# Kernel tuning notes

Hardware: AMD Instinct MI355X
Metric: run time of the kernel (lower is better)

The kernel has to match this reference:

```python
import jax, jax.numpy as jnp
import numpy as np
from jax import lax

N_NODES = 64; N_GROUPS = 16; GROUP_SIZE = 4
B = 256; L = 64; CNN_C = 32; GH = 128; DH = 128; OUT = 64
E1 = 262144; E2 = 32768
GROUP_NODES = jnp.arange(N_NODES).reshape(N_GROUPS, GROUP_SIZE)

PARAM_SHAPES = [
    ('conv_w3', (N_NODES, CNN_C, 3)), ('conv_b3', (N_NODES, CNN_C)),
    ('conv_w5', (N_NODES, CNN_C, 5)), ('conv_b5', (N_NODES, CNN_C)),
    ('conv_w7', (N_NODES, CNN_C, 7)), ('conv_b7', (N_NODES, CNN_C)),
    ('tconv_w3', (N_NODES, CNN_C, 3)), ('tconv_b3', (N_NODES, CNN_C)),
    ('tconv_w5', (N_NODES, CNN_C, 5)), ('tconv_b5', (N_NODES, CNN_C)),
    ('tconv_w7', (N_NODES, CNN_C, 7)), ('tconv_b7', (N_NODES, CNN_C)),
    ('ff_w', (N_NODES, 6 * CNN_C, GH)), ('ff_b', (N_NODES, GH)),
    ('lower_w', (GH, GH)), ('lower_b', (GH,)),
    ('upper_w', (GH, GH)), ('upper_b', (GH,)),
    ('agg_w', (N_GROUPS, GROUP_SIZE * GH, GH)), ('agg_b', (N_GROUPS, GH)),
    ('disc_w', (N_GROUPS, 2 * GH, DH)), ('disc_b', (N_GROUPS, DH)),
    ('fc_w', (N_GROUPS * DH, OUT)), ('fc_b', (OUT,)),
]


def setup_inputs() -> dict:
    key = jax.random.key(0)
    ks = jax.random.split(key, 6 + len(PARAM_SHAPES))
    d = {
        'x1': jax.random.normal(ks[0], (B * N_NODES, 4, L), jnp.float32),
        'x2': jax.random.normal(ks[1], (B * N_NODES, 4, L), jnp.float32),
        'edge_index1': jax.random.randint(ks[2], (2, E1), 0, B * N_NODES),
        'edge_index2': jax.random.randint(ks[3], (2, E1), 0, B * N_NODES),
        'group_edge_index1': jax.random.randint(ks[4], (2, E2), 0, B * N_GROUPS),
        'group_edge_index2': jax.random.randint(ks[5], (2, E2), 0, B * N_GROUPS),
    }
    for i, (name, shape) in enumerate(PARAM_SHAPES):
        d[name] = jax.random.normal(ks[6 + i], shape, jnp.float32) * 0.05
    return d


def _grouped_conv_max(x, w, b, pad):
    # x: [B, N, Lx] (one input channel per node), w: [N, C, k], b: [N, C]
    N, C, k = w.shape
    y = lax.conv_general_dilated(x, w.reshape(N * C, 1, k), (1,), [(pad, pad)],
                                 feature_group_count=N,
                                 dimension_numbers=('NCH', 'OIH', 'NCH'))
    y = y + b.reshape(1, N * C, 1)
    return y.max(axis=2).reshape(x.shape[0], N, C)  # max over time per channel


def _gcn(x, edge_index, W, bias):
    # PyG GCNConv: add self loops, symmetric D^-1/2 (A+I) D^-1/2 normalization
    n = x.shape[0]
    loops = jnp.arange(n)
    src = jnp.concatenate([edge_index[0], loops])
    dst = jnp.concatenate([edge_index[1], loops])
    deg = jax.ops.segment_sum(jnp.ones(src.shape[0], x.dtype), dst, n)
    dinv = jnp.where(deg > 0, lax.rsqrt(deg), 0.0)
    h = x @ W
    msg = h[src] * (dinv[src] * dinv[dst])[:, None]
    return jax.ops.segment_sum(msg, dst, n) + bias


def reference(x1, x2, edge_index1, edge_index2, group_edge_index1, group_edge_index2,
              conv_w3, conv_b3, conv_w5, conv_b5, conv_w7, conv_b7,
              tconv_w3, tconv_b3, tconv_w5, tconv_b5, tconv_w7, tconv_b7,
              ff_w, ff_b, lower_w, lower_b, upper_w, upper_b,
              agg_w, agg_b, disc_w, disc_b, fc_w, fc_b):
    def encode(x, ei, gei):
        xr = x.reshape(B, N_NODES, 4, L)  # row = b*N_NODES + n -> x[n::N] == xr[:, n]
        feats = jnp.concatenate([
            _grouped_conv_max(xr[:, :, 0, :], conv_w3, conv_b3, 1),
            _grouped_conv_max(xr[:, :, 0, :], conv_w5, conv_b5, 2),
            _grouped_conv_max(xr[:, :, 0, :], conv_w7, conv_b7, 3),
            _grouped_conv_max(xr[:, :, 1, :-2], tconv_w3, tconv_b3, 1),
            _grouped_conv_max(xr[:, :, 2, :-4], tconv_w5, tconv_b5, 2),
            _grouped_conv_max(xr[:, :, 3, :-6], tconv_w7, tconv_b7, 3),
        ], axis=2)  # [B, N, 6C]
        feats = jax.nn.relu(feats)
        h = jax.nn.relu(jnp.einsum('bnf,nfh->bnh', feats, ff_w) + ff_b)  # per-node Linear
        h = _gcn(h.reshape(B * N_NODES, GH), ei, lower_w, lower_b)
        hg = h.reshape(B, N_NODES, GH)[:, GROUP_NODES]  # [B, G, S, GH]
        hg = hg.reshape(B, N_GROUPS, GROUP_SIZE * GH)
        hg = jnp.einsum('bgf,gfh->bgh', hg, agg_w) + agg_b  # per-group aggregate Linear
        hg = _gcn(hg.reshape(B * N_GROUPS, GH), gei, upper_w, upper_b)
        return jax.nn.relu(hg).reshape(B, N_GROUPS, GH)

    h1 = encode(x1, edge_index1, group_edge_index1)
    h2 = encode(x2, edge_index2, group_edge_index2)
    d = jnp.concatenate([h1, h2], axis=2)  # [B, G, 2*GH]
    d = jax.nn.relu(jnp.einsum('bgf,gfd->bgd', d, disc_w) + disc_b)  # per-group disc fc
    return d.reshape(B, N_GROUPS * DH) @ fc_w + fc_b  # [B, OUT]
```

## Files before the change

kernel.cpp:

```cpp
#include <hip/hip_runtime.h>
#include <hip/hip_bf16.h>

namespace {

constexpr int Bn      = 256;
constexpr int NNODES  = 64;
constexpr int NGROUPS = 16;
constexpr int L       = 64;
constexpr int C       = 32;
constexpr int GH      = 128;
constexpr int E1      = 262144;
constexpr int E2      = 32768;
constexpr int NROWS   = Bn * NNODES;
constexpr int GROWS   = Bn * NGROUPS;
constexpr int XROW    = 296;

template<int K, int LX>
__device__ __forceinline__ void convmax2(const float* __restrict__ xin_al,
                                         const float* __restrict__ wpa,
                                         const float* __restrict__ wpb,
                                         float& ma, float& mb)
{
    constexpr int PAD = (K - 1) / 2;
    constexpr int OFF = 3 - PAD;
    float wa[K], wb[K];
    #pragma unroll
    for (int i = 0; i < K; ++i) { wa[i] = wpa[i]; wb[i] = wpb[i]; }
    ma = -3.0e38f; mb = -3.0e38f;
    #pragma unroll
    for (int p0 = 0; p0 < LX; p0 += 16) {
        float xw[24];
        #pragma unroll
        for (int q = 0; q < 6; ++q) {
            const float4 v = *(const float4*)(xin_al + p0 + q * 4);
            xw[q * 4 + 0] = v.x; xw[q * 4 + 1] = v.y;
            xw[q * 4 + 2] = v.z; xw[q * 4 + 3] = v.w;
        }
        #pragma unroll
        for (int p = 0; p < 16; p += 2) {
            if (p0 + p + 1 < LX) {
                float sa0 = 0.f, sb0 = 0.f, sa1 = 0.f, sb1 = 0.f;
                #pragma unroll
                for (int i = 0; i < K; ++i) {
                    const float xv0 = xw[p + OFF + i];
                    const float xv1 = xw[p + 1 + OFF + i];
                    sa0 = fmaf(wa[i], xv0, sa0);
                    sb0 = fmaf(wb[i], xv0, sb0);
                    sa1 = fmaf(wa[i], xv1, sa1);
                    sb1 = fmaf(wb[i], xv1, sb1);
                }
                ma = fmaxf(fmaxf(sa0, sa1), ma);
                mb = fmaxf(fmaxf(sb0, sb1), mb);
            }
        }
    }
}

__device__ __forceinline__ void conv6_ch0(
    const float* __restrict__ xin_al,
    const float* __restrict__ w3a, const float* __restrict__ w3b,
    const float* __restrict__ w5a, const float* __restrict__ w5b,
    const float* __restrict__ w7a, const float* __restrict__ w7b,
    float& m3a, float& m3b, float& m5a, float& m5b, float& m7a, float& m7b)
{
    float a3[3], b3[3], a5[5], b5[5], a7[7], b7[7];
    #pragma unroll
    for (int i = 0; i < 3; ++i) { a3[i] = w3a[i]; b3[i] = w3b[i]; }
    #pragma unroll
    for (int i = 0; i < 5; ++i) { a5[i] = w5a[i]; b5[i] = w5b[i]; }
    #pragma unroll
    for (int i = 0; i < 7; ++i) { a7[i] = w7a[i]; b7[i] = w7b[i]; }
    m3a = m3b = m5a = m5b = m7a = m7b = -3.0e38f;
    #pragma unroll
    for (int p0 = 0; p0 < 64; p0 += 16) {
        float xw[24];
        #pragma unroll
        for (int q = 0; q < 6; ++q) {
            const float4 v = *(const float4*)(xin_al + p0 + q * 4);
            xw[q * 4 + 0] = v.x; xw[q * 4 + 1] = v.y;
            xw[q * 4 + 2] = v.z; xw[q * 4 + 3] = v.w;
        }
        #pragma unroll
        for (int p = 0; p < 16; p += 2) {
            float s3a0 = 0.f, s3b0 = 0.f, s3a1 = 0.f, s3b1 = 0.f;
            #pragma unroll
            for (int i = 0; i < 3; ++i) {
                const float xv0 = xw[p + 2 + i], xv1 = xw[p + 3 + i];
                s3a0 = fmaf(a3[i], xv0, s3a0); s3b0 = fmaf(b3[i], xv0, s3b0);
                s3a1 = fmaf(a3[i], xv1, s3a1); s3b1 = fmaf(b3[i], xv1, s3b1);
            }
            m3a = fmaxf(fmaxf(s3a0, s3a1), m3a);
            m3b = fmaxf(fmaxf(s3b0, s3b1), m3b);
            float s5a0 = 0.f, s5b0 = 0.f, s5a1 = 0.f, s5b1 = 0.f;
            #pragma unroll
            for (int i = 0; i < 5; ++i) {
                const float xv0 = xw[p + 1 + i], xv1 = xw[p + 2 + i];
                s5a0 = fmaf(a5[i], xv0, s5a0); s5b0 = fmaf(b5[i], xv0, s5b0);
                s5a1 = fmaf(a5[i], xv1, s5a1); s5b1 = fmaf(b5[i], xv1, s5b1);
            }
            m5a = fmaxf(fmaxf(s5a0, s5a1), m5a);
            m5b = fmaxf(fmaxf(s5b0, s5b1), m5b);
            float s7a0 = 0.f, s7b0 = 0.f, s7a1 = 0.f, s7b1 = 0.f;
            #pragma unroll
            for (int i = 0; i < 7; ++i) {
                const float xv0 = xw[p + 0 + i], xv1 = xw[p + 1 + i];
                s7a0 = fmaf(a7[i], xv0, s7a0); s7b0 = fmaf(b7[i], xv0, s7b0);
                s7a1 = fmaf(a7[i], xv1, s7a1); s7b1 = fmaf(b7[i], xv1, s7b1);
            }
            m7a = fmaxf(fmaxf(s7a0, s7a1), m7a);
            m7b = fmaxf(fmaxf(s7b0, s7b1), m7b);
        }
    }
}

__global__ __launch_bounds__(256) void k_conv_feats(
    const float* __restrict__ x1, const float* __restrict__ x2,
    const float* __restrict__ w3,  const float* __restrict__ b3,
    const float* __restrict__ w5,  const float* __restrict__ b5,
    const float* __restrict__ w7,  const float* __restrict__ b7,
    const float* __restrict__ tw3, const float* __restrict__ tb3,
    const float* __restrict__ tw5, const float* __restrict__ tb5,
    const float* __restrict__ tw7, const float* __restrict__ tb7,
    float* __restrict__ feats)
{
    __shared__ float xs[16 * XROW];
    const int t = threadIdx.x;
    const int eb = blockIdx.x >> 10;
    const float* __restrict__ x = eb ? x2 : x1;
    const int row0 = (blockIdx.x & 1023) * 16;
    for (int idx = t; idx < 16 * 4 * 72; idx += 256) {
        const int r   = idx / 288;
        const int rem = idx - r * 288;
        const int c   = rem / 72;
        const int j   = rem - c * 72;
        const int l   = j - 3;
        float v = 0.f;
        if (l >= 0 && l < 64 - 2 * c)
            v = x[(size_t)(row0 + r) * 256 + c * 64 + l];
        xs[r * XROW + c * 72 + j] = v;
    }
    __syncthreads();

    const int rr  = t >> 4;
    const int cp  = t & 15;
    const int ch0 = cp * 2;
    const int row = row0 + rr;
    const int n   = row & (NNODES - 1);
    const int wc0 = n * C + ch0;
    const int wc1 = wc0 + 1;
    const float* xb0 = &xs[rr * XROW + 0 * 72];
    const float* xb1 = &xs[rr * XROW + 1 * 72];
    const float* xb2 = &xs[rr * XROW + 2 * 72];
    const float* xb3 = &xs[rr * XROW + 3 * 72];

    float* o = feats + (size_t)(eb * NROWS + row) * 192 + ch0;

    float m3a, m3b, m5a, m5b, m7a, m7b;
    conv6_ch0(xb0, w3 + wc0 * 3, w3 + wc1 * 3, w5 + wc0 * 5, w5 + wc1 * 5,
              w7 + wc0 * 7, w7 + wc1 * 7, m3a, m3b, m5a, m5b, m7a, m7b);
    *(float2*)(o + 0 * 32) = make_float2(fmaxf(m3a + b3[wc0], 0.f), fmaxf(m3b + b3[wc1], 0.f));
    *(float2*)(o + 1 * 32) = make_float2(fmaxf(m5a + b5[wc0], 0.f), fmaxf(m5b + b5[wc1], 0.f));
    *(float2*)(o + 2 * 32) = make_float2(fmaxf(m7a + b7[wc0], 0.f), fmaxf(m7b + b7[wc1], 0.f));

    float ma, mb;
    convmax2<3, 62>(xb1, tw3 + wc0 * 3, tw3 + wc1 * 3, ma, mb);
    *(float2*)(o + 3 * 32) = make_float2(fmaxf(ma + tb3[wc0], 0.f), fmaxf(mb + tb3[wc1], 0.f));
    convmax2<5, 60>(xb2, tw5 + wc0 * 5, tw5 + wc1 * 5, ma, mb);
    *(float2*)(o + 4 * 32) = make_float2(fmaxf(ma + tb5[wc0], 0.f), fmaxf(mb + tb5[wc1], 0.f));
    convmax2<7, 58>(xb3, tw7 + wc0 * 7, tw7 + wc1 * 7, ma, mb);
    *(float2*)(o + 5 * 32) = make_float2(fmaxf(ma + tb7[wc0], 0.f), fmaxf(mb + tb7[wc1], 0.f));
}

__global__ __launch_bounds__(256) void k_ff_lower(
    const float* __restrict__ feats, const float* __restrict__ ffw,
    const float* __restrict__ ffb, const float* __restrict__ lw,
    float* __restrict__ hw)
{
    const int nb = blockIdx.x >> 6;
    const int n  = blockIdx.x & 63;
    const int t  = threadIdx.x;
    const int o  = t & 127;
    const int rh = t >> 7;
    __shared__ float fs[16 * 192];
    __shared__ float h0s[16 * 128];
    {
        float4* d4 = (float4*)fs;
        for (int i = t; i < 16 * 48; i += 256) {
            const int r = i / 48, c4 = i - r * 48;
            d4[i] = *(const float4*)(feats + ((size_t)(nb * 16 + r) * 64 + n) * 192 + c4 * 4);
        }
    }
    __syncthreads();
    {
        const float* w = ffw + (size_t)n * 192 * 128 + o;
        float acc[8];
        #pragma unroll
        for (int r = 0; r < 8; ++r) acc[r] = 0.f;
        #pragma unroll 2
        for (int f = 0; f < 192; f += 4) {
            const float w0 = w[(f + 0) * 128];
            const float w1 = w[(f + 1) * 128];
            const float w2 = w[(f + 2) * 128];
            const float w3_ = w[(f + 3) * 128];
            #pragma unroll
            for (int r = 0; r < 8; ++r) {
                const float4 xv = *(const float4*)(fs + (rh * 8 + r) * 192 + f);
                acc[r] = fmaf(xv.x, w0, acc[r]);
                acc[r] = fmaf(xv.y, w1, acc[r]);
                acc[r] = fmaf(xv.z, w2, acc[r]);
                acc[r] = fmaf(xv.w, w3_, acc[r]);
            }
        }
        const float bias = ffb[n * 128 + o];
        #pragma unroll
        for (int r = 0; r < 8; ++r)
            h0s[(rh * 8 + r) * 128 + o] = fmaxf(acc[r] + bias, 0.f);
    }
    __syncthreads();
    {
        const float* w = lw + o;
        float acc[8];
        #pragma unroll
        for (int r = 0; r < 8; ++r) acc[r] = 0.f;
        #pragma unroll 2
        for (int f = 0; f < 128; f += 4) {
            const float w0 = w[(f + 0) * 128];
            const float w1 = w[(f + 1) * 128];
            const float w2 = w[(f + 2) * 128];
            const float w3_ = w[(f + 3) * 128];
            #pragma unroll
            for (int r = 0; r < 8; ++r) {
                const float4 xv = *(const float4*)(h0s + (rh * 8 + r) * 128 + f);
                acc[r] = fmaf(xv.x, w0, acc[r]);
                acc[r] = fmaf(xv.y, w1, acc[r]);
                acc[r] = fmaf(xv.z, w2, acc[r]);
                acc[r] = fmaf(xv.w, w3_, acc[r]);
            }
        }
        #pragma unroll
        for (int r = 0; r < 8; ++r) {
            const int row = nb * 16 + rh * 8 + r;
            hw[((size_t)row * 64 + n) * 128 + o] = acc[r];
        }
    }
}

__global__ __launch_bounds__(256) void k_gemm128(
    const float* __restrict__ X, const float* __restrict__ W,
    float* __restrict__ Y)
{
    const int r0 = blockIdx.x * 16;
    const int t  = threadIdx.x;
    const int o  = t & 127;
    const int rh = t >> 7;
    __shared__ float xs[16 * 128];
    {
        float4* d4 = (float4*)xs;
        const float4* s4 = (const float4*)(X + (size_t)r0 * 128);
        for (int i = t; i < 512; i += 256) d4[i] = s4[i];
    }
    __syncthreads();
    const float* w = W + o;
    float acc[8];
    #pragma unroll
    for (int r = 0; r < 8; ++r) acc[r] = 0.f;
    #pragma unroll 2
    for (int f = 0; f < 128; f += 4) {
        const float w0 = w[(f + 0) * 128];
        const float w1 = w[(f + 1) * 128];
        const float w2 = w[(f + 2) * 128];
        const float w3_ = w[(f + 3) * 128];
        #pragma unroll
        for (int r = 0; r < 8; ++r) {
            const float4 xv = *(const float4*)(xs + (rh * 8 + r) * 128 + f);
            acc[r] = fmaf(xv.x, w0, acc[r]);
            acc[r] = fmaf(xv.y, w1, acc[r]);
            acc[r] = fmaf(xv.z, w2, acc[r]);
            acc[r] = fmaf(xv.w, w3_, acc[r]);
        }
    }
    #pragma unroll
    for (int r = 0; r < 8; ++r)
        Y[(size_t)(r0 + rh * 8 + r) * 128 + o] = acc[r];
}

__global__ void k_zero_i(int* __restrict__ p, int n) {
    const int i = blockIdx.x * blockDim.x + threadIdx.x;
    if (i < n) p[i] = 0;
}
__global__ void k_hist_all(const int* __restrict__ ei0, const int* __restrict__ ei1,
                           const int* __restrict__ gei0, const int* __restrict__ gei1,
                           int* __restrict__ cnt1, int* __restrict__ cnt2)
{
    const int gid = blockIdx.x * blockDim.x + threadIdx.x;
    if (gid < 2 * E1) {
        const int eb = gid >= E1;
        const int le = gid - (eb ? E1 : 0);
        const int* ei = eb ? ei1 : ei0;
        atomicAdd(&cnt1[(eb ? NROWS : 0) + ei[E1 + le]], 1);
    } else {
        const int g2 = gid - 2 * E1;
        const int eb = g2 >= E2;
        const int le = g2 - (eb ? E2 : 0);
        const int* ei = eb ? gei1 : gei0;
        atomicAdd(&cnt2[(eb ? GROWS : 0) + ei[E2 + le]], 1);
    }
}
__global__ __launch_bounds__(256) void k_scan_bsum_all(
    const int* __restrict__ cnt1, const int* __restrict__ cnt2,
    int* __restrict__ bsum1, int* __restrict__ bsum2)
{
    const int blk = blockIdx.x, t = threadIdx.x;
    const int* cnt; int* bsum; int lblk;
    if (blk < 32) { cnt = cnt1; bsum = bsum1; lblk = blk; }
    else          { cnt = cnt2; bsum = bsum2; lblk = blk - 32; }
    const int4 v = ((const int4*)cnt)[lblk * 256 + t];
    int s = v.x + v.y + v.z + v.w;
    #pragma unroll
    for (int off = 32; off > 0; off >>= 1) s += __shfl_down(s, off);
    __shared__ int wsum[4];
    if ((t & 63) == 0) wsum[t >> 6] = s;
    __syncthreads();
    if (t == 0) bsum[lblk] = wsum[0] + wsum[1] + wsum[2] + wsum[3];
}
__global__ __launch_bounds__(256) void k_scan_final_all(
    const int* __restrict__ cnt1, const int* __restrict__ bsum1,
    int* __restrict__ offs1, int* __restrict__ cur1, float* __restrict__ dinv1,
    const int* __restrict__ cnt2, const int* __restrict__ bsum2,
    int* __restrict__ offs2, int* __restrict__ cur2, float* __restrict__ dinv2)
{
    const int blk = blockIdx.x, t = threadIdx.x;
    const int* cnt; const int* bsum; int* offs; int* cur; float* dinv;
    int n, nb, lblk;
    if (blk < 32) { cnt = cnt1; bsum = bsum1; offs = offs1; cur = cur1; dinv = dinv1;
                    n = 2 * NROWS; nb = 32; lblk = blk; }
    else          { cnt = cnt2; bsum = bsum2; offs = offs2; cur = cur2; dinv = dinv2;
                    n = 2 * GROWS; nb = 8; lblk = blk - 32; }
    int base = 0;
    for (int i = 0; i < lblk; ++i) base += bsum[i];
    const int4 v = ((const int4*)cnt)[lblk * 256 + t];
    const int s = v.x + v.y + v.z + v.w;
    int sc = s;
    #pragma unroll
    for (int off = 1; off < 64; off <<= 1) {
        const int u = __shfl_up(sc, off);
        if ((t & 63) >= off) sc += u;
    }
    __shared__ int wsum[4];
    if ((t & 63) == 63) wsum[t >> 6] = sc;
    __syncthreads();
    int wbase = 0;
    for (int wv = 0; wv < (t >> 6); ++wv) wbase += wsum[wv];
    int o0 = base + wbase + sc - s;
    const int gi = lblk * 1024 + t * 4;
    offs[gi + 0] = o0; cur[gi + 0] = o0; dinv[gi + 0] = rsqrtf(1.f + (float)v.x); o0 += v.x;
    offs[gi + 1] = o0; cur[gi + 1] = o0; dinv[gi + 1] = rsqrtf(1.f + (float)v.y); o0 += v.y;
    offs[gi + 2] = o0; cur[gi + 2] = o0; dinv[gi + 2] = rsqrtf(1.f + (float)v.z); o0 += v.z;
    offs[gi + 3] = o0; cur[gi + 3] = o0; dinv[gi + 3] = rsqrtf(1.f + (float)v.w); o0 += v.w;
    if (lblk == nb - 1 && t == 255) offs[n] = o0;
}
__global__ void k_fill_all(const int* __restrict__ ei0, const int* __restrict__ ei1,
                           const int* __restrict__ gei0, const int* __restrict__ gei1,
                           int* __restrict__ cur1, int* __restrict__ esrc1,
                           int* __restrict__ cur2, int* __restrict__ esrc2)
{
    const int gid = blockIdx.x * blockDim.x + threadIdx.x;
    if (gid < 2 * E1) {
        const int eb = gid >= E1;
        const int le = gid - (eb ? E1 : 0);
        const int* ei = eb ? ei1 : ei0;
        const int s = ei[le];
        const int d = ei[E1 + le];
        const int pos = atomicAdd(&cur1[(eb ? NROWS : 0) + d], 1);
        esrc1[pos] = s;
    } else {
        const int g2 = gid - 2 * E1;
        const int eb = g2 >= E2;
        const int le = g2 - (eb ? E2 : 0);
        const int* ei = eb ? gei1 : gei0;
        const int s = ei[le];
        const int d = ei[E2 + le];
        const int pos = atomicAdd(&cur2[(eb ? GROWS : 0) + d], 1);
        esrc2[pos] = s;
    }
}

__global__ __launch_bounds__(128) void k_gcn_gather(
    const int* __restrict__ offs, const int* __restrict__ esrc,
    const float* __restrict__ hw, const float* __restrict__ dinv,
    const float* __restrict__ bias, float* __restrict__ out, int n)
{
    const int d = blockIdx.x;
    const int t = threadIdx.x;
    const int sbase = (d >= n) ? n : 0;
    const int e0 = offs[d], e1 = offs[d + 1];
    const float dd = dinv[d];
    float a0 = hw[(size_t)d * 128 + t] * dd;
    float a1 = 0.f, a2 = 0.f, a3 = 0.f;
    int j = e0;
    for (; j + 3 < e1; j += 4) {
        const int s0 = sbase + esrc[j],     s1 = sbase + esrc[j + 1];
        const int s2 = sbase + esrc[j + 2], s3 = sbase + esrc[j + 3];
        a0 = fmaf(hw[(size_t)s0 * 128 + t], dinv[s0], a0);
        a1 = fmaf(hw[(size_t)s1 * 128 + t], dinv[s1], a1);
        a2 = fmaf(hw[(size_t)s2 * 128 + t], dinv[s2], a2);
        a3 = fmaf(hw[(size_t)s3 * 128 + t], dinv[s3], a3);
    }
    for (; j < e1; ++j) {
        const int s = sbase + esrc[j];
        a0 = fmaf(hw[(size_t)s * 128 + t], dinv[s], a0);
    }
    const float acc = (a0 + a1) + (a2 + a3);
    out[(size_t)d * 128 + t] = fmaf(acc, dd, bias[t]);
}

__global__ __launch_bounds__(256) void k_agg(
    const float* __restrict__ h, const float* __restrict__ aggw,
    const float* __restrict__ aggb, float* __restrict__ hg)
{
    const int bt = blockIdx.x >> 4;
    const int g  = blockIdx.x & 15;
    const int t  = threadIdx.x;
    const int o  = t & 127;
    const int kk = t >> 7;
    __shared__ float fs[4 * 512];
    __shared__ float red[2][4][128];
    {
        const int b0 = bt * 4;
        float4* dst = (float4*)fs;
        for (int i = t; i < 4 * 128; i += 256) {
            const int r = i >> 7;
            const int q = i & 127;
            dst[i] = *(const float4*)(h + ((size_t)(b0 + r) * 64 + g * 4) * 128 + q * 4);
        }
    }
    __syncthreads();
    const float* w = aggw + (size_t)g * 512 * 128 + (size_t)kk * 256 * 128 + o;
    float a0 = 0.f, a1 = 0.f, a2 = 0.f, a3 = 0.f;
    const float* x0 = fs + 0 * 512 + kk * 256;
    const float* x1 = fs + 1 * 512 + kk * 256;
    const float* x2 = fs + 2 * 512 + kk * 256;
    const float* x3 = fs + 3 * 512 + kk * 256;
    #pragma unroll 8
    for (int f = 0; f < 256; ++f) {
        const float wv = w[f * 128];
        a0 = fmaf(x0[f], wv, a0);
        a1 = fmaf(x1[f], wv, a1);
        a2 = fmaf(x2[f], wv, a2);
        a3 = fmaf(x3[f], wv, a3);
    }
    red[kk][0][o] = a0; red[kk][1][o] = a1; red[kk][2][o] = a2; red[kk][3][o] = a3;
    __syncthreads();
    if (t < 128) {
        const float bias = aggb[g * 128 + t];
        #pragma unroll
        for (int r = 0; r < 4; ++r) {
            const int b = bt * 4 + r;
            hg[((size_t)b * 16 + g) * 128 + t] = red[0][r][t] + red[1][r][t] + bias;
        }
    }
}

__global__ __launch_bounds__(256) void k_disc(
    const float* __restrict__ h1, const float* __restrict__ h2,
    const float* __restrict__ dw, const float* __restrict__ db,
    float* __restrict__ dd)
{
    const int bt = blockIdx.x >> 4;
    const int g  = blockIdx.x & 15;
    const int t  = threadIdx.x;
    const int o  = t & 127;
    const int kk = t >> 7;
    __shared__ float fs[4 * 256];
    __shared__ float red[2][4][128];
    {
        const int half = t >> 7;
        #pragma unroll
        for (int r = 0; r < 4; ++r) {
            const int rowi = ((bt * 4 + r) * 16 + g);
            const float* src = half ? h2 : h1;
            fs[r * 256 + half * 128 + o] = fmaxf(src[(size_t)rowi * 128 + o], 0.f);
        }
    }
    __syncthreads();
    const float* w = dw + (size_t)g * 256 * 128 + (size_t)kk * 128 * 128 + o;
    float a0 = 0.f, a1 = 0.f, a2 = 0.f, a3 = 0.f;
    const float* x0 = fs + 0 * 256 + kk * 128;
    const float* x1 = fs + 1 * 256 + kk * 128;
    const float* x2 = fs + 2 * 256 + kk * 128;
    const float* x3 = fs + 3 * 256 + kk * 128;
    #pragma unroll 8
    for (int f = 0; f < 128; ++f) {
        const float wv = w[f * 128];
        a0 = fmaf(x0[f], wv, a0);
        a1 = fmaf(x1[f], wv, a1);
        a2 = fmaf(x2[f], wv, a2);
        a3 = fmaf(x3[f], wv, a3);
    }
    red[kk][0][o] = a0; red[kk][1][o] = a1; red[kk][2][o] = a2; red[kk][3][o] = a3;
    __syncthreads();
    if (t < 128) {
        const float bias = db[g * 128 + t];
        #pragma unroll
        for (int r = 0; r < 4; ++r) {
            const int b = bt * 4 + r;
            dd[(size_t)b * 2048 + g * 128 + t] =
                fmaxf(red[0][r][t] + red[1][r][t] + bias, 0.f);
        }
    }
}

__global__ __launch_bounds__(256) void k_fc(
    const float* __restrict__ dd, const float* __restrict__ fcw,
    const float* __restrict__ fcb, float* __restrict__ out)
{
    const int b = blockIdx.x;
    const int t = threadIdx.x;
    const int o = t & 63;
    const int k = t >> 6;
    __shared__ float ds[2048];
    __shared__ float red[4][64];
    for (int i = t; i < 2048; i += 256) ds[i] = dd[(size_t)b * 2048 + i];
    __syncthreads();
    const float* w  = fcw + (k * 512) * 64 + o;
    const float* xr = ds + k * 512;
    float a0 = 0.f, a1 = 0.f, a2 = 0.f, a3 = 0.f;
    #pragma unroll 4
    for (int f = 0; f < 512; f += 4) {
        a0 = fmaf(xr[f + 0], w[(f + 0) * 64], a0);
        a1 = fmaf(xr[f + 1], w[(f + 1) * 64], a1);
        a2 = fmaf(xr[f + 2], w[(f + 2) * 64], a2);
        a3 = fmaf(xr[f + 3], w[(f + 3) * 64], a3);
    }
    red[k][o] = (a0 + a1) + (a2 + a3);
    __syncthreads();
    if (t < 64)
        out[(size_t)b * 64 + t] = ((red[0][t] + red[1][t]) + (red[2][t] + red[3][t])) + fcb[t];
}

}

extern "C" void kernel_launch(void* const* d_in, const int* in_sizes, int n_in,
                              void* d_out, int out_size, void* d_ws, size_t ws_size,
                              hipStream_t stream)
{
    const float* x1 = (const float*)d_in[0];
    const float* x2 = (const float*)d_in[1];
    const int* ei0  = (const int*)d_in[2];
    const int* ei1  = (const int*)d_in[3];
    const int* gei0 = (const int*)d_in[4];
    const int* gei1 = (const int*)d_in[5];
    const float* conv_w3 = (const float*)d_in[6];
    const float* conv_b3 = (const float*)d_in[7];
    const float* conv_w5 = (const float*)d_in[8];
    const float* conv_b5 = (const float*)d_in[9];
    const float* conv_w7 = (const float*)d_in[10];
    const float* conv_b7 = (const float*)d_in[11];
    const float* tconv_w3 = (const float*)d_in[12];
    const float* tconv_b3 = (const float*)d_in[13];
    const float* tconv_w5 = (const float*)d_in[14];
    const float* tconv_b5 = (const float*)d_in[15];
    const float* tconv_w7 = (const float*)d_in[16];
    const float* tconv_b7 = (const float*)d_in[17];
    const float* ff_w    = (const float*)d_in[18];
    const float* ff_b    = (const float*)d_in[19];
    const float* lower_w = (const float*)d_in[20];
    const float* lower_b = (const float*)d_in[21];
    const float* upper_w = (const float*)d_in[22];
    const float* upper_b = (const float*)d_in[23];
    const float* agg_w   = (const float*)d_in[24];
    const float* agg_b   = (const float*)d_in[25];
    const float* disc_w  = (const float*)d_in[26];
    const float* disc_b  = (const float*)d_in[27];
    const float* fc_w    = (const float*)d_in[28];
    const float* fc_b    = (const float*)d_in[29];

    float* ws = (float*)d_ws;
    float* f_feats = ws;
    float* f_hw    = ws + 10485760;
    float* f_gout  = ws + 14680064;
    float* f_hg    = ws + 18874368;
    float* f_hgw   = ws + 19922944;
    float* f_henc  = ws + 20971520;
    float* f_dd    = ws + 22020096;
    float* f_dinv1 = ws + 22544384;
    float* f_dinv2 = ws + 22577152;
    int* ip    = (int*)(ws + 22585344);
    int* cnt1  = ip;
    int* cnt2  = cnt1 + 2 * NROWS;
    int* offs1 = cnt2 + 2 * GROWS;
    int* cur1  = offs1 + 2 * NROWS + 1;
    int* esrc1 = cur1 + 2 * NROWS;
    int* offs2 = esrc1 + 2 * E1;
    int* cur2  = offs2 + 2 * GROWS + 1;
    int* esrc2 = cur2 + 2 * GROWS;
    int* bsum1 = esrc2 + 2 * E2;
    int* bsum2 = bsum1 + 32;

    k_zero_i<<<(2 * NROWS + 2 * GROWS) / 256, 256, 0, stream>>>(cnt1, 2 * NROWS + 2 * GROWS);
    k_hist_all<<<(2 * E1 + 2 * E2) / 256, 256, 0, stream>>>(ei0, ei1, gei0, gei1, cnt1, cnt2);
    k_scan_bsum_all<<<40, 256, 0, stream>>>(cnt1, cnt2, bsum1, bsum2);
    k_scan_final_all<<<40, 256, 0, stream>>>(cnt1, bsum1, offs1, cur1, f_dinv1,
                                             cnt2, bsum2, offs2, cur2, f_dinv2);
    k_fill_all<<<(2 * E1 + 2 * E2) / 256, 256, 0, stream>>>(ei0, ei1, gei0, gei1,
                                                            cur1, esrc1, cur2, esrc2);

    k_conv_feats<<<2 * NROWS / 16, 256, 0, stream>>>(x1, x2,
        conv_w3, conv_b3, conv_w5, conv_b5, conv_w7, conv_b7,
        tconv_w3, tconv_b3, tconv_w5, tconv_b5, tconv_w7, tconv_b7, f_feats);
    k_ff_lower<<<2048, 256, 0, stream>>>(f_feats, ff_w, ff_b, lower_w, f_hw);
    k_gcn_gather<<<2 * NROWS, 128, 0, stream>>>(offs1, esrc1, f_hw, f_dinv1,
                                                lower_b, f_gout, NROWS);
    k_agg<<<2 * (Bn / 4) * 16, 256, 0, stream>>>(f_gout, agg_w, agg_b, f_hg);
    k_gemm128<<<2 * GROWS / 16, 256, 0, stream>>>(f_hg, upper_w, f_hgw);
    k_gcn_gather<<<2 * GROWS, 128, 0, stream>>>(offs2, esrc2, f_hgw, f_dinv2,
                                                upper_b, f_henc, GROWS);

    k_disc<<<(Bn / 4) * 16, 256, 0, stream>>>(f_henc, f_henc + (size_t)GROWS * 128,
                                              disc_w, disc_b, f_dd);
    k_fc<<<Bn, 256, 0, stream>>>(f_dd, fc_w, fc_b, (float*)d_out);
}
```

Before: 283.1 us.

## Fuse lower GCN gather, group aggregate and upper GEMM; fuse upper gather with disc

The lower-graph GCN gather, the per-group aggregate linear and the upper_w GEMM are merged into one kernel that keeps intermediate rows in shared memory. The upper-graph gather is likewise merged with the discriminator linear layer. This removes several launches and the global round-trips of f_gout, f_hg and f_henc. In exchange, each block now gathers 16 (or 8) destination rows serially with only 256 threads, so the latency-bound gather has less parallelism and may see worse load balance.

```diff
diff --git a/kernel.cpp b/kernel.cpp
--- a/kernel.cpp
+++ b/kernel.cpp
@@ -245,45 +245,6 @@
     }
 }
 
-__global__ __launch_bounds__(256) void k_gemm128(
-    const float* __restrict__ X, const float* __restrict__ W,
-    float* __restrict__ Y)
-{
-    const int r0 = blockIdx.x * 16;
-    const int t  = threadIdx.x;
-    const int o  = t & 127;
-    const int rh = t >> 7;
-    __shared__ float xs[16 * 128];
-    {
-        float4* d4 = (float4*)xs;
-        const float4* s4 = (const float4*)(X + (size_t)r0 * 128);
-        for (int i = t; i < 512; i += 256) d4[i] = s4[i];
-    }
-    __syncthreads();
-    const float* w = W + o;
-    float acc[8];
-    #pragma unroll
-    for (int r = 0; r < 8; ++r) acc[r] = 0.f;
-    #pragma unroll 2
-    for (int f = 0; f < 128; f += 4) {
-        const float w0 = w[(f + 0) * 128];
-        const float w1 = w[(f + 1) * 128];
-        const float w2 = w[(f + 2) * 128];
-        const float w3_ = w[(f + 3) * 128];
-        #pragma unroll
-        for (int r = 0; r < 8; ++r) {
-            const float4 xv = *(const float4*)(xs + (rh * 8 + r) * 128 + f);
-            acc[r] = fmaf(xv.x, w0, acc[r]);
-            acc[r] = fmaf(xv.y, w1, acc[r]);
-            acc[r] = fmaf(xv.z, w2, acc[r]);
-            acc[r] = fmaf(xv.w, w3_, acc[r]);
-        }
-    }
-    #pragma unroll
-    for (int r = 0; r < 8; ++r)
-        Y[(size_t)(r0 + rh * 8 + r) * 128 + o] = acc[r];
-}
-
 __global__ void k_zero_i(int* __restrict__ p, int n) {
     const int i = blockIdx.x * blockDim.x + threadIdx.x;
     if (i < n) p[i] = 0;
@@ -385,84 +346,107 @@
     }
 }
 
-__global__ __launch_bounds__(128) void k_gcn_gather(
+__global__ __launch_bounds__(256) void k_gau(
     const int* __restrict__ offs, const int* __restrict__ esrc,
     const float* __restrict__ hw, const float* __restrict__ dinv,
-    const float* __restrict__ bias, float* __restrict__ out, int n)
-{
-    const int d = blockIdx.x;
-    const int t = threadIdx.x;
-    const int sbase = (d >= n) ? n : 0;
-    const int e0 = offs[d], e1 = offs[d + 1];
-    const float dd = dinv[d];
-    float a0 = hw[(size_t)d * 128 + t] * dd;
-    float a1 = 0.f, a2 = 0.f, a3 = 0.f;
-    int j = e0;
-    for (; j + 3 < e1; j += 4) {
-        const int s0 = sbase + esrc[j],     s1 = sbase + esrc[j + 1];
-        const int s2 = sbase + esrc[j + 2], s3 = sbase + esrc[j + 3];
-        a0 = fmaf(hw[(size_t)s0 * 128 + t], dinv[s0], a0);
-        a1 = fmaf(hw[(size_t)s1 * 128 + t], dinv[s1], a1);
-        a2 = fmaf(hw[(size_t)s2 * 128 + t], dinv[s2], a2);
-        a3 = fmaf(hw[(size_t)s3 * 128 + t], dinv[s3], a3);
-    }
-    for (; j < e1; ++j) {
-        const int s = sbase + esrc[j];
-        a0 = fmaf(hw[(size_t)s * 128 + t], dinv[s], a0);
-    }
-    const float acc = (a0 + a1) + (a2 + a3);
-    out[(size_t)d * 128 + t] = fmaf(acc, dd, bias[t]);
-}
-
-__global__ __launch_bounds__(256) void k_agg(
-    const float* __restrict__ h, const float* __restrict__ aggw,
-    const float* __restrict__ aggb, float* __restrict__ hg)
+    const float* __restrict__ lb,
+    const float* __restrict__ aggw, const float* __restrict__ aggb,
+    const float* __restrict__ uw, float* __restrict__ hgw)
 {
     const int bt = blockIdx.x >> 4;
     const int g  = blockIdx.x & 15;
     const int t  = threadIdx.x;
     const int o  = t & 127;
-    const int kk = t >> 7;
-    __shared__ float fs[4 * 512];
+    const int hf = t >> 7;
+    __shared__ float fsA[2][16][128];
+    __shared__ float fsB[4][512];
     __shared__ float red[2][4][128];
+    __shared__ float hgs[4][128];
+
+    const int Bp0 = bt * 4;
+    const int eb  = (Bp0 >= 256) ? 1 : 0;
+    const int sbase = eb ? NROWS : 0;
+    const int blocal0 = Bp0 - (eb ? 256 : 0);
+
+    for (int r = 0; r < 16; ++r) {
+        const int bi = r >> 2, j = r & 3;
+        const int drow = sbase + (blocal0 + bi) * 64 + g * 4 + j;
+        const int e0 = offs[drow], e1 = offs[drow + 1];
+        float acc  = (hf == 0) ? hw[(size_t)drow * 128 + o] * dinv[drow] : 0.f;
+        float acc2 = 0.f;
+        int jj = e0 + hf;
+        for (; jj + 2 < e1; jj += 4) {
+            const int s0 = sbase + esrc[jj];
+            const int s1 = sbase + esrc[jj + 2];
+            acc  = fmaf(hw[(size_t)s0 * 128 + o], dinv[s0], acc);
+            acc2 = fmaf(hw[(size_t)s1 * 128 + o], dinv[s1], acc2);
+        }
+        for (; jj < e1; jj += 2) {
+            const int s = sbase + esrc[jj];
+            acc = fmaf(hw[(size_t)s * 128 + o], dinv[s], acc);
+        }
+        fsA[hf][r][o] = acc + acc2;
+    }
+    __syncthreads();
+    for (int idx = t; idx < 2048; idx += 256) {
+        const int r = idx >> 7, oc = idx & 127;
+        const int bi = r >> 2, j = r & 3;
+        const int drow = sbase + (blocal0 + bi) * 64 + g * 4 + j;
+        fsB[bi][j * 128 + oc] =
+            fmaf(fsA[0][r][oc] + fsA[1][r][oc], dinv[drow], lb[oc]);
+    }
+    __syncthreads();
     {
-        const int b0 = bt * 4;
-        float4* dst = (float4*)fs;
-        for (int i = t; i < 4 * 128; i += 256) {
-            const int r = i >> 7;
-            const int q = i & 127;
-            dst[i] = *(const float4*)(h + ((size_t)(b0 + r) * 64 + g * 4) * 128 + q * 4);
-        }
-    }
-    __syncthreads();
-    const float* w = aggw + (size_t)g * 512 * 128 + (size_t)kk * 256 * 128 + o;
-    float a0 = 0.f, a1 = 0.f, a2 = 0.f, a3 = 0.f;
-    const float* x0 = fs + 0 * 512 + kk * 256;
-    const float* x1 = fs + 1 * 512 + kk * 256;
-    const float* x2 = fs + 2 * 512 + kk * 256;
-    const float* x3 = fs + 3 * 512 + kk * 256;
-    #pragma unroll 8
-    for (int f = 0; f < 256; ++f) {
-        const float wv = w[f * 128];
-        a0 = fmaf(x0[f], wv, a0);
-        a1 = fmaf(x1[f], wv, a1);
-        a2 = fmaf(x2[f], wv, a2);
-        a3 = fmaf(x3[f], wv, a3);
-    }
-    red[kk][0][o] = a0; red[kk][1][o] = a1; red[kk][2][o] = a2; red[kk][3][o] = a3;
+        const float* w = aggw + (size_t)g * 512 * 128 + (size_t)hf * 256 * 128 + o;
+        float a0 = 0.f, a1 = 0.f, a2 = 0.f, a3 = 0.f;
+        const float* x0 = &fsB[0][hf * 256];
+        const float* x1 = &fsB[1][hf * 256];
+        const float* x2 = &fsB[2][hf * 256];
+        const float* x3 = &fsB[3][hf * 256];
+        #pragma unroll 8
+        for (int f = 0; f < 256; ++f) {
+            const float wv = w[f * 128];
+            a0 = fmaf(x0[f], wv, a0);
+            a1 = fmaf(x1[f], wv, a1);
+            a2 = fmaf(x2[f], wv, a2);
+            a3 = fmaf(x3[f], wv, a3);
+        }
+        red[hf][0][o] = a0; red[hf][1][o] = a1; red[hf][2][o] = a2; red[hf][3][o] = a3;
+    }
     __syncthreads();
     if (t < 128) {
         const float bias = aggb[g * 128 + t];
         #pragma unroll
-        for (int r = 0; r < 4; ++r) {
-            const int b = bt * 4 + r;
-            hg[((size_t)b * 16 + g) * 128 + t] = red[0][r][t] + red[1][r][t] + bias;
-        }
-    }
-}
-
-__global__ __launch_bounds__(256) void k_disc(
-    const float* __restrict__ h1, const float* __restrict__ h2,
+        for (int r = 0; r < 4; ++r)
+            hgs[r][t] = red[0][r][t] + red[1][r][t] + bias;
+    }
+    __syncthreads();
+    {
+        const float* w = uw + o;
+        float a0 = 0.f, a1 = 0.f;
+        #pragma unroll 2
+        for (int f = 0; f < 128; f += 4) {
+            const float w0 = w[(f + 0) * 128];
+            const float w1 = w[(f + 1) * 128];
+            const float w2 = w[(f + 2) * 128];
+            const float w3_ = w[(f + 3) * 128];
+            const float4 xv0 = *(const float4*)(&hgs[hf * 2 + 0][f]);
+            const float4 xv1 = *(const float4*)(&hgs[hf * 2 + 1][f]);
+            a0 = fmaf(xv0.x, w0, a0); a0 = fmaf(xv0.y, w1, a0);
+            a0 = fmaf(xv0.z, w2, a0); a0 = fmaf(xv0.w, w3_, a0);
+            a1 = fmaf(xv1.x, w0, a1); a1 = fmaf(xv1.y, w1, a1);
+            a1 = fmaf(xv1.z, w2, a1); a1 = fmaf(xv1.w, w3_, a1);
+        }
+        const int r0g = eb * GROWS + (blocal0 + hf * 2) * 16 + g;
+        hgw[(size_t)r0g * 128 + o] = a0;
+        hgw[(size_t)(r0g + 16) * 128 + o] = a1;
+    }
+}
+
+__global__ __launch_bounds__(256) void k_gdisc(
+    const int* __restrict__ offs, const int* __restrict__ esrc,
+    const float* __restrict__ hgw, const float* __restrict__ dinv,
+    const float* __restrict__ ub,
     const float* __restrict__ dw, const float* __restrict__ db,
     float* __restrict__ dd)
 {
@@ -470,34 +454,58 @@
     const int g  = blockIdx.x & 15;
     const int t  = threadIdx.x;
     const int o  = t & 127;
-    const int kk = t >> 7;
-    __shared__ float fs[4 * 256];
+    const int hf = t >> 7;
+    __shared__ float fsA[2][8][128];
+    __shared__ float fs[4][256];
     __shared__ float red[2][4][128];
+
+    for (int r = 0; r < 8; ++r) {
+        const int bi = r >> 1, eb = r & 1;
+        const int sbase = eb ? GROWS : 0;
+        const int drow = sbase + (bt * 4 + bi) * 16 + g;
+        const int e0 = offs[drow], e1 = offs[drow + 1];
+        float acc  = (hf == 0) ? hgw[(size_t)drow * 128 + o] * dinv[drow] : 0.f;
+        float acc2 = 0.f;
+        int jj = e0 + hf;
+        for (; jj + 2 < e1; jj += 4) {
+            const int s0 = sbase + esrc[jj];
+            const int s1 = sbase + esrc[jj + 2];
+            acc  = fmaf(hgw[(size_t)s0 * 128 + o], dinv[s0], acc);
+            acc2 = fmaf(hgw[(size_t)s1 * 128 + o], dinv[s1], acc2);
+        }
+        for (; jj < e1; jj += 2) {
+            const int s = sbase + esrc[jj];
+            acc = fmaf(hgw[(size_t)s * 128 + o], dinv[s], acc);
+        }
+        fsA[hf][r][o] = acc + acc2;
+    }
+    __syncthreads();
+    for (int idx = t; idx < 1024; idx += 256) {
+        const int r = idx >> 7, oc = idx & 127;
+        const int bi = r >> 1, eb = r & 1;
+        const int sbase = eb ? GROWS : 0;
+        const int drow = sbase + (bt * 4 + bi) * 16 + g;
+        fs[bi][eb * 128 + oc] =
+            fmaxf(fmaf(fsA[0][r][oc] + fsA[1][r][oc], dinv[drow], ub[oc]), 0.f);
+    }
+    __syncthreads();
     {
-        const int half = t >> 7;
-        #pragma unroll
-        for (int r = 0; r < 4; ++r) {
-            const int rowi = ((bt * 4 + r) * 16 + g);
-            const float* src = half ? h2 : h1;
-            fs[r * 256 + half * 128 + o] = fmaxf(src[(size_t)rowi * 128 + o], 0.f);
-        }
-    }
-    __syncthreads();
-    const float* w = dw + (size_t)g * 256 * 128 + (size_t)kk * 128 * 128 + o;
-    float a0 = 0.f, a1 = 0.f, a2 = 0.f, a3 = 0.f;
-    const float* x0 = fs + 0 * 256 + kk * 128;
-    const float* x1 = fs + 1 * 256 + kk * 128;
-    const float* x2 = fs + 2 * 256 + kk * 128;
-    const float* x3 = fs + 3 * 256 + kk * 128;
-    #pragma unroll 8
-    for (int f = 0; f < 128; ++f) {
-        const float wv = w[f * 128];
-        a0 = fmaf(x0[f], wv, a0);
-        a1 = fmaf(x1[f], wv, a1);
-        a2 = fmaf(x2[f], wv, a2);
-        a3 = fmaf(x3[f], wv, a3);
-    }
-    red[kk][0][o] = a0; red[kk][1][o] = a1; red[kk][2][o] = a2; red[kk][3][o] = a3;
+        const float* w = dw + (size_t)g * 256 * 128 + (size_t)hf * 128 * 128 + o;
+        float a0 = 0.f, a1 = 0.f, a2 = 0.f, a3 = 0.f;
+        const float* x0 = &fs[0][hf * 128];
+        const float* x1 = &fs[1][hf * 128];
+        const float* x2 = &fs[2][hf * 128];
+        const float* x3 = &fs[3][hf * 128];
+        #pragma unroll 8
+        for (int f = 0; f < 128; ++f) {
+            const float wv = w[f * 128];
+            a0 = fmaf(x0[f], wv, a0);
+            a1 = fmaf(x1[f], wv, a1);
+            a2 = fmaf(x2[f], wv, a2);
+            a3 = fmaf(x3[f], wv, a3);
+        }
+        red[hf][0][o] = a0; red[hf][1][o] = a1; red[hf][2][o] = a2; red[hf][3][o] = a3;
+    }
     __syncthreads();
     if (t < 128) {
         const float bias = db[g * 128 + t];
@@ -578,10 +586,7 @@
     float* ws = (float*)d_ws;
     float* f_feats = ws;
     float* f_hw    = ws + 10485760;
-    float* f_gout  = ws + 14680064;
-    float* f_hg    = ws + 18874368;
     float* f_hgw   = ws + 19922944;
-    float* f_henc  = ws + 20971520;
     float* f_dd    = ws + 22020096;
     float* f_dinv1 = ws + 22544384;
     float* f_dinv2 = ws + 22577152;
@@ -609,14 +614,9 @@
         conv_w3, conv_b3, conv_w5, conv_b5, conv_w7, conv_b7,
         tconv_w3, tconv_b3, tconv_w5, tconv_b5, tconv_w7, tconv_b7, f_feats);
     k_ff_lower<<<2048, 256, 0, stream>>>(f_feats, ff_w, ff_b, lower_w, f_hw);
-    k_gcn_gather<<<2 * NROWS, 128, 0, stream>>>(offs1, esrc1, f_hw, f_dinv1,
-                                                lower_b, f_gout, NROWS);
-    k_agg<<<2 * (Bn / 4) * 16, 256, 0, stream>>>(f_gout, agg_w, agg_b, f_hg);
-    k_gemm128<<<2 * GROWS / 16, 256, 0, stream>>>(f_hg, upper_w, f_hgw);
-    k_gcn_gather<<<2 * GROWS, 128, 0, stream>>>(offs2, esrc2, f_hgw, f_dinv2,
-                                                upper_b, f_henc, GROWS);
-
-    k_disc<<<(Bn / 4) * 16, 256, 0, stream>>>(f_henc, f_henc + (size_t)GROWS * 128,
-                                              disc_w, disc_b, f_dd);
+    k_gau<<<2048, 256, 0, stream>>>(offs1, esrc1, f_hw, f_dinv1, lower_b,
+                                    agg_w, agg_b, upper_w, f_hgw);
+    k_gdisc<<<1024, 256, 0, stream>>>(offs2, esrc2, f_hgw, f_dinv2, upper_b,
+                                      disc_w, disc_b, f_dd);
     k_fc<<<Bn, 256, 0, stream>>>(f_dd, fc_w, fc_b, (float*)d_out);
 }
```

Result: slower. 343.8 us (+21.4%).
